# Optimization experiments

Measured on AMD Instinct MI355X. Metric: run time of the kernel, lower is better.

## Reference

```python
import jax, jax.numpy as jnp
import numpy as np

COMMITMENT_COST = 0.25


def setup_inputs() -> dict:
    key = jax.random.key(0)
    k1, k2 = jax.random.split(key)
    z = jax.random.normal(k1, (32, 256, 32, 32), dtype=jnp.float32)
    # codebook init matches torch uniform_(-1/codebook_size, 1/codebook_size)
    embedding = jax.random.uniform(k2, (1024, 256), dtype=jnp.float32,
                                   minval=-1.0 / 1024, maxval=1.0 / 1024)
    return {"z": z, "embedding": embedding}


def reference(z, embedding):
    # z: [B, C, H, W] -> [B, H, W, C]
    z_bhwc = jnp.transpose(z.astype(jnp.float32), (0, 2, 3, 1))
    B, H, W, C = z_bhwc.shape
    z_flat = z_bhwc.reshape(-1, C)                      # [N, C]

    # squared-distance matrix via norms + matmul: [N, K]
    d = (jnp.sum(z_flat ** 2, axis=1, keepdims=True)
         + jnp.sum(embedding ** 2, axis=1)
         - 2.0 * jnp.einsum('nc,kc->nk', z_flat, embedding))

    min_encoding_indices = jnp.argmin(d, axis=1)        # [N]
    z_quantized = embedding[min_encoding_indices].reshape(B, H, W, C)

    commitment_loss = COMMITMENT_COST * (jax.lax.stop_gradient(z_quantized) - z_bhwc) ** 2
    codebook_loss = (z_quantized - jax.lax.stop_gradient(z_bhwc)) ** 2
    loss = commitment_loss + codebook_loss              # [B, H, W, C]

    # straight-through estimator
    z_quantized = z_bhwc + jax.lax.stop_gradient(z_quantized - z_bhwc)
    z_quantized = jnp.transpose(z_quantized, (0, 3, 1, 2))  # [B, C, H, W]
    return z_quantized, loss, min_encoding_indices
```

## Files before the change

### kernel.cpp

```cpp
#include <hip/hip_runtime.h>

#define ZC     256
#define KCODES 1024
#define MARGIN 4e-4f
#define WIN    1e-4f

typedef __attribute__((ext_vector_type(4))) float f32x4;
typedef __attribute__((ext_vector_type(8))) short s16x8;
typedef unsigned int u32t;
typedef u32t __attribute__((address_space(1))) as1_u32;
typedef u32t __attribute__((address_space(3))) as3_u32;

__device__ __forceinline__ void glds16(const void* g, void* l) {
    __builtin_amdgcn_global_load_lds((const as1_u32*)g, (as3_u32*)l, 16, 0, 0);
}
__device__ __forceinline__ unsigned short bf16_rn(float x) {
    union { float f; u32t u; } v; v.f = x;
    return (unsigned short)((v.u + 0x7FFFu + ((v.u >> 16) & 1u)) >> 16);
}

__global__ __launch_bounds__(256)
void vq_prep_z(const float* __restrict__ z, unsigned short* __restrict__ Ab)
{
    const int t = threadIdx.x, blk = blockIdx.x;
    const int pt = (blk >> 3) * 64 + (t & 63);
    const int c0 = (blk & 7) * 32 + (t >> 6) * 8;
    const int b = pt >> 10, hw = pt & 1023;
    const float* zp = z + (size_t)b * (ZC * 1024) + (size_t)c0 * 1024 + hw;

    unsigned short hi[8];
    #pragma unroll
    for (int j = 0; j < 8; ++j) hi[j] = bf16_rn(zp[(size_t)j * 1024]);
    uint4 ph;
    ph.x = (u32t)hi[0] | ((u32t)hi[1] << 16); ph.y = (u32t)hi[2] | ((u32t)hi[3] << 16);
    ph.z = (u32t)hi[4] | ((u32t)hi[5] << 16); ph.w = (u32t)hi[6] | ((u32t)hi[7] << 16);

    const size_t kb = (size_t)(c0 >> 6);
    const int sw = (c0 & 63) ^ ((pt & 7) << 3);
    *reinterpret_cast<uint4*>(Ab + kb * (32768ull * 64) + (size_t)pt * 64 + sw) = ph;
}

__global__ __launch_bounds__(256)
void vq_prep_e(const float* __restrict__ emb, unsigned short* __restrict__ Bb)
{
    const int t = threadIdx.x, blk = blockIdx.x;
    const int code = (blk >> 3) * 64 + (t & 63);
    const int c0 = (blk & 7) * 32 + (t >> 6) * 8;
    const float* ep = emb + (size_t)code * ZC + c0;

    unsigned short hi[8];
    #pragma unroll
    for (int j = 0; j < 8; ++j) hi[j] = bf16_rn(ep[j]);
    uint4 ph;
    ph.x = (u32t)hi[0] | ((u32t)hi[1] << 16); ph.y = (u32t)hi[2] | ((u32t)hi[3] << 16);
    ph.z = (u32t)hi[4] | ((u32t)hi[5] << 16); ph.w = (u32t)hi[6] | ((u32t)hi[7] << 16);

    const size_t kb = (size_t)(c0 >> 6);
    const int sw = (c0 & 63) ^ ((code & 7) << 3);
    *reinterpret_cast<uint4*>(Bb + kb * (1024ull * 64) + (size_t)code * 64 + sw) = ph;
}

__global__ __launch_bounds__(256)
void vq_ens_np(const float* __restrict__ emb, float* __restrict__ ens_np,
               int* __restrict__ cnt)
{
    if (blockIdx.x == 0 && threadIdx.x == 0) *cnt = 0;
    const int t = threadIdx.x, g = t >> 3, r = t & 7;
    const int code = blockIdx.x * 32 + g;
    const float* er = emb + (size_t)code * ZC;

    float lo, hi;
    {
        const float a0 = er[r], a1 = er[128 + r];
        lo = __fmul_rn(a0, a0); hi = __fmul_rn(a1, a1);
    }
    #pragma unroll
    for (int i = 1; i < 16; ++i) {
        const int c = 8 * i + r;
        const float a0 = er[c], a1 = er[128 + c];
        lo = __fadd_rn(lo, __fmul_rn(a0, a0));
        hi = __fadd_rn(hi, __fmul_rn(a1, a1));
    }
    #pragma unroll
    for (int mk = 1; mk < 8; mk <<= 1) {
        lo = __fadd_rn(lo, __shfl_xor(lo, mk));
        hi = __fadd_rn(hi, __shfl_xor(hi, mk));
    }
    if (r == 0) ens_np[code] = __fadd_rn(lo, hi);
}

__global__ __launch_bounds__(256, 2)
void vq_gemm_argmin(const unsigned short* __restrict__ Ab,
                    const unsigned short* __restrict__ Bb,
                    const float* __restrict__ ens_g, float* __restrict__ out_idx)
{
    __shared__ unsigned short As[64 * 64];
    __shared__ unsigned short Bs[128 * 64];

    const int t = threadIdx.x;
    const int lane = t & 63, wv = t >> 6;
    const int col = lane & 15, kg = lane >> 4;
    const int pt0 = blockIdx.x * 64;
    const int kx = (col & 7) << 3;

    int aoff[4][2], boff[2][2];
    #pragma unroll
    for (int m = 0; m < 4; ++m)
        #pragma unroll
        for (int s = 0; s < 2; ++s)
            aoff[m][s] = (m * 16 + col) * 64 + ((s * 32 + kg * 8) ^ kx);
    #pragma unroll
    for (int n = 0; n < 2; ++n)
        #pragma unroll
        for (int s = 0; s < 2; ++s)
            boff[n][s] = (wv * 32 + n * 16 + col) * 64 + ((s * 32 + kg * 8) ^ kx);

    f32x4 acc[4][2];
    #pragma unroll
    for (int m = 0; m < 4; ++m)
        #pragma unroll
        for (int n = 0; n < 2; ++n) acc[m][n] = (f32x4){0.f, 0.f, 0.f, 0.f};

    float v1[16], v2[16]; int id1[16];
    #pragma unroll
    for (int i = 0; i < 16; ++i) { v1[i] = 3.4e38f; v2[i] = 3.4e38f; id1[i] = 0; }

    for (int ct = 0; ct < 8; ++ct) {
        for (int ks = 0; ks < 4; ++ks) {
            const char* aS = (const char*)(Ab + (size_t)ks * 2097152ull + (size_t)pt0 * 64);
            const char* bS = (const char*)(Bb + (size_t)ks * 65536ull + (size_t)ct * 8192);

            __syncthreads();
            glds16(aS + t * 16,        (char*)As + t * 16);
            glds16(aS + 4096 + t * 16, (char*)As + 4096 + t * 16);
            #pragma unroll
            for (int q = 0; q < 4; ++q)
                glds16(bS + q * 4096 + t * 16, (char*)Bs + q * 4096 + t * 16);
            __syncthreads();

            s16x8 af[4][2], bf[2][2];
            #pragma unroll
            for (int m = 0; m < 4; ++m)
                #pragma unroll
                for (int s = 0; s < 2; ++s)
                    af[m][s] = *reinterpret_cast<const s16x8*>(As + aoff[m][s]);
            #pragma unroll
            for (int n = 0; n < 2; ++n)
                #pragma unroll
                for (int s = 0; s < 2; ++s)
                    bf[n][s] = *reinterpret_cast<const s16x8*>(Bs + boff[n][s]);
            #pragma unroll
            for (int m = 0; m < 4; ++m)
                #pragma unroll
                for (int n = 0; n < 2; ++n) {
                    acc[m][n] = __builtin_amdgcn_mfma_f32_16x16x32_bf16(af[m][0], bf[n][0], acc[m][n], 0, 0, 0);
                    acc[m][n] = __builtin_amdgcn_mfma_f32_16x16x32_bf16(af[m][1], bf[n][1], acc[m][n], 0, 0, 0);
                }

            if (ks == 3) {
                #pragma unroll
                for (int n = 0; n < 2; ++n) {
                    const int code = ct * 128 + wv * 32 + n * 16 + col;
                    const float en = ens_g[code];
                    #pragma unroll
                    for (int m = 0; m < 4; ++m)
                        #pragma unroll
                        for (int j = 0; j < 4; ++j) {
                            const float sc = fmaf(-2.f, acc[m][n][j], en);
                            const int sl = m * 4 + j;
                            if (sc < v1[sl]) { v2[sl] = v1[sl]; v1[sl] = sc; id1[sl] = code; }
                            else if (sc < v2[sl]) { v2[sl] = sc; }
                            acc[m][n][j] = 0.f;
                        }
                }
            }
        }
    }

    float w1[16], w2[16]; int wid[16];
    #pragma unroll
    for (int sl = 0; sl < 16; ++sl) {
        float a1 = v1[sl]; int ai = id1[sl]; float a2 = v2[sl];
        #pragma unroll
        for (int mk = 1; mk < 16; mk <<= 1) {
            const float o1 = __shfl_xor(a1, mk);
            const int   oi = __shfl_xor(ai, mk);
            const float o2 = __shfl_xor(a2, mk);
            if (o1 < a1)      { a2 = fminf(a1, o2); a1 = o1; ai = oi; }
            else if (o1 > a1) { a2 = fminf(a2, o1); }
            else              { a2 = (oi != ai) ? a1 : fminf(a2, o2); ai = (oi < ai) ? oi : ai; }
        }
        w1[sl] = a1; w2[sl] = a2; wid[sl] = ai;
    }

    __syncthreads();
    float* mv1 = reinterpret_cast<float*>(As);
    float* mv2 = mv1 + 256;
    int*   mid = reinterpret_cast<int*>(mv2 + 256);
    if (col == 0) {
        #pragma unroll
        for (int sl = 0; sl < 16; ++sl) {
            const int m = sl >> 2, j = sl & 3;
            const int p = m * 16 + kg * 4 + j;
            mv1[wv * 64 + p] = w1[sl];
            mv2[wv * 64 + p] = w2[sl];
            mid[wv * 64 + p] = wid[sl];
        }
    }
    __syncthreads();
    if (t < 64) {
        float a1 = mv1[t], a2 = mv2[t]; int ai = mid[t];
        #pragma unroll
        for (int w = 1; w < 4; ++w) {
            const float b1 = mv1[w * 64 + t], b2 = mv2[w * 64 + t];
            const int   bi = mid[w * 64 + t];
            if (b1 < a1)      { a2 = fminf(a1, b2); a1 = b1; ai = bi; }
            else if (b1 > a1) { a2 = fminf(a2, b1); }
            else              { a2 = a1; ai = (bi < ai) ? bi : ai; }
        }
        out_idx[pt0 + t] = ((a2 - a1) <= MARGIN) ? (-1.0f - (float)ai) : (float)ai;
    }
}

__global__ __launch_bounds__(256)
void vq_compact(const float* __restrict__ idxf, int* __restrict__ cnt,
                int* __restrict__ list)
{
    const int n = blockIdx.x * 256 + threadIdx.x;
    if (idxf[n] < 0.f) { const int p = atomicAdd(cnt, 1); list[p] = n; }
}

__global__ __launch_bounds__(256, 1)
void vq_fixup6(const float* __restrict__ z, const float* __restrict__ emb,
               const float* __restrict__ ens_np, float* __restrict__ idxf,
               const int* __restrict__ cnt, const int* __restrict__ list)
{
    __shared__ float  zsb[4 * 264];
    __shared__ float  scr[4 * 1024];
    __shared__ float  znv[4];
    __shared__ float  smin[4];
    __shared__ int    pn[4];
    __shared__ float  redm[4];
    __shared__ int    candk[128];
    __shared__ int    candp[128];
    __shared__ int    ccnt;
    __shared__ double dred[4];
    __shared__ float  bestd_s[4];
    __shared__ int    bestk_s[4];

    const int t = threadIdx.x;
    const int g = t >> 3, r = t & 7;
    const int C = *cnt;
    const int base = blockIdx.x * 4;
    if (base >= C) return;
    const int npts = (C - base < 4) ? (C - base) : 4;

    if (t < 4) pn[t] = (base + t < C) ? list[base + t] : list[base];
    if (t == 0) ccnt = 0;
    __syncthreads();
    #pragma unroll
    for (int p = 0; p < 4; ++p) {
        const int n = pn[p];
        const int b = n >> 10, q = n & 1023;
        zsb[p * 264 + t] = z[(size_t)b * (ZC * 1024) + (size_t)t * 1024 + q];
    }
    __syncthreads();

    if (t < 32) {
        const float* zp = zsb + g * 264;
        float lo = __fmul_rn(zp[r], zp[r]);
        float hi = __fmul_rn(zp[128 + r], zp[128 + r]);
        #pragma unroll
        for (int i = 1; i < 16; ++i) {
            const int c = 8 * i + r;
            lo = __fadd_rn(lo, __fmul_rn(zp[c], zp[c]));
            hi = __fadd_rn(hi, __fmul_rn(zp[128 + c], zp[128 + c]));
        }
        #pragma unroll
        for (int mk = 1; mk < 8; mk <<= 1) {
            lo = __fadd_rn(lo, __shfl_xor(lo, mk));
            hi = __fadd_rn(hi, __shfl_xor(hi, mk));
        }
        if (r == 0) znv[g] = __fadd_rn(lo, hi);
    }

    const float* zb0 = zsb + 0 * 264 + r * 4;
    const float* zb1 = zsb + 1 * 264 + r * 4;
    const float* zb2 = zsb + 2 * 264 + r * 4;
    const float* zb3 = zsb + 3 * 264 + r * 4;

    float4 eA0, eA1, eA2, eA3, eA4, eA5, eA6, eA7;
    {
        const float* er = emb + (size_t)g * ZC + r * 4;
        eA0 = *reinterpret_cast<const float4*>(er);
        eA1 = *reinterpret_cast<const float4*>(er + 32);
        eA2 = *reinterpret_cast<const float4*>(er + 64);
        eA3 = *reinterpret_cast<const float4*>(er + 96);
        eA4 = *reinterpret_cast<const float4*>(er + 128);
        eA5 = *reinterpret_cast<const float4*>(er + 160);
        eA6 = *reinterpret_cast<const float4*>(er + 192);
        eA7 = *reinterpret_cast<const float4*>(er + 224);
    }

    for (int tile = 0; tile < 32; ++tile) {
        float4 eB0, eB1, eB2, eB3, eB4, eB5, eB6, eB7;
        if (tile < 31) {
            const float* er = emb + (size_t)(tile + 1) * 32 * ZC + (size_t)g * ZC + r * 4;
            eB0 = *reinterpret_cast<const float4*>(er);
            eB1 = *reinterpret_cast<const float4*>(er + 32);
            eB2 = *reinterpret_cast<const float4*>(er + 64);
            eB3 = *reinterpret_cast<const float4*>(er + 96);
            eB4 = *reinterpret_cast<const float4*>(er + 128);
            eB5 = *reinterpret_cast<const float4*>(er + 160);
            eB6 = *reinterpret_cast<const float4*>(er + 192);
            eB7 = *reinterpret_cast<const float4*>(er + 224);
        }

        float s0 = 0.f, s1 = 0.f, s2 = 0.f, s3 = 0.f;
        #define SCREEN_STEP(EV, OFF)                                           \
        {                                                                      \
            const float4 a0 = *reinterpret_cast<const float4*>(zb0 + (OFF));   \
            const float4 a1 = *reinterpret_cast<const float4*>(zb1 + (OFF));   \
            const float4 a2 = *reinterpret_cast<const float4*>(zb2 + (OFF));   \
            const float4 a3 = *reinterpret_cast<const float4*>(zb3 + (OFF));   \
            s0 = fmaf(EV.x, a0.x, s0); s0 = fmaf(EV.y, a0.y, s0);              \
            s0 = fmaf(EV.z, a0.z, s0); s0 = fmaf(EV.w, a0.w, s0);              \
            s1 = fmaf(EV.x, a1.x, s1); s1 = fmaf(EV.y, a1.y, s1);              \
            s1 = fmaf(EV.z, a1.z, s1); s1 = fmaf(EV.w, a1.w, s1);              \
            s2 = fmaf(EV.x, a2.x, s2); s2 = fmaf(EV.y, a2.y, s2);              \
            s2 = fmaf(EV.z, a2.z, s2); s2 = fmaf(EV.w, a2.w, s2);              \
            s3 = fmaf(EV.x, a3.x, s3); s3 = fmaf(EV.y, a3.y, s3);              \
            s3 = fmaf(EV.z, a3.z, s3); s3 = fmaf(EV.w, a3.w, s3);              \
        }
        SCREEN_STEP(eA0, 0)
        SCREEN_STEP(eA1, 32)
        SCREEN_STEP(eA2, 64)
        SCREEN_STEP(eA3, 96)
        SCREEN_STEP(eA4, 128)
        SCREEN_STEP(eA5, 160)
        SCREEN_STEP(eA6, 192)
        SCREEN_STEP(eA7, 224)
        #undef SCREEN_STEP

        #pragma unroll
        for (int mk = 1; mk < 8; mk <<= 1) {
            s0 += __shfl_xor(s0, mk);
            s1 += __shfl_xor(s1, mk);
            s2 += __shfl_xor(s2, mk);
            s3 += __shfl_xor(s3, mk);
        }
        if (r == 0) {
            const int code = tile * 32 + g;
            const float en = ens_np[code];
            scr[0 * 1024 + code] = fmaf(-2.f, s0, en);
            scr[1 * 1024 + code] = fmaf(-2.f, s1, en);
            scr[2 * 1024 + code] = fmaf(-2.f, s2, en);
            scr[3 * 1024 + code] = fmaf(-2.f, s3, en);
        }

        eA0 = eB0; eA1 = eB1; eA2 = eB2; eA3 = eB3;
        eA4 = eB4; eA5 = eB5; eA6 = eB6; eA7 = eB7;
    }
    __syncthreads();

    for (int p = 0; p < 4; ++p) {
        float m = fminf(fminf(scr[p * 1024 + t],       scr[p * 1024 + t + 256]),
                        fminf(scr[p * 1024 + t + 512], scr[p * 1024 + t + 768]));
        #pragma unroll
        for (int mk = 1; mk < 64; mk <<= 1) m = fminf(m, __shfl_xor(m, mk));
        if ((t & 63) == 0) redm[t >> 6] = m;
        __syncthreads();
        if (t == 0) smin[p] = fminf(fminf(redm[0], redm[1]), fminf(redm[2], redm[3]));
        __syncthreads();
    }

    for (int p = 0; p < 4; ++p) {
        #pragma unroll
        for (int rep = 0; rep < 4; ++rep) {
            const int code = rep * 256 + t;
            if (scr[p * 1024 + code] <= smin[p] + WIN) {
                const int pos = atomicAdd(&ccnt, 1);
                if (pos < 128) { candk[pos] = code; candp[pos] = p; }
            }
        }
    }
    __syncthreads();
    const int NC = (ccnt < 128) ? ccnt : 128;

    if (t < 4) { bestd_s[t] = 3.4e38f; bestk_s[t] = 0x7fffffff; }
    __syncthreads();
    for (int ci = 0; ci < NC; ++ci) {
        const int code = candk[ci], p = candp[ci];
        double dd = (double)emb[(size_t)code * ZC + t] * (double)zsb[p * 264 + t];
        #pragma unroll
        for (int mk = 1; mk < 64; mk <<= 1) dd = dd + __shfl_xor(dd, mk);
        if ((t & 63) == 0) dred[t >> 6] = dd;
        __syncthreads();
        if (t == 0) {
            const double tot = (dred[0] + dred[1]) + (dred[2] + dred[3]);
            const float t2f = (float)tot;
            const float d = __fsub_rn(__fadd_rn(znv[p], ens_np[code]),
                                      __fmul_rn(2.0f, t2f));
            if (d < bestd_s[p] || (d == bestd_s[p] && code < bestk_s[p])) {
                bestd_s[p] = d; bestk_s[p] = code;
            }
        }
        __syncthreads();
    }
    if (t < npts) idxf[pn[t]] = (float)bestk_s[t];
}

__global__ __launch_bounds__(256)
void vq_outputs_kernel(const float* __restrict__ z, const float* __restrict__ emb,
                       const float* __restrict__ idxf,
                       float* __restrict__ out_q, float* __restrict__ out_loss)
{
    __shared__ float zts[32 * 257];
    __shared__ int   ids[32];

    const int t  = threadIdx.x;
    const int bh = blockIdx.x;
    const int b  = bh >> 5, h = bh & 31;
    const int n0 = bh * 32;

    if (t < 32) ids[t] = (int)idxf[n0 + t];
    __syncthreads();

    const size_t zbase = (size_t)b * (ZC * 1024) + h * 32;

    for (int rep = 0; rep < 32; ++rep) {
        const int flat = rep * 256 + t;
        const int c = flat >> 5;
        const int ww = flat & 31;
        const size_t ga = zbase + (size_t)c * 1024 + ww;
        const float zv = z[ga];
        zts[ww * 257 + c] = zv;
        out_q[ga] = emb[(size_t)ids[ww] * ZC + c];
    }
    __syncthreads();

    for (int rep = 0; rep < 32; ++rep) {
        const float e = emb[(size_t)ids[rep] * ZC + t];
        const float d = e - zts[rep * 257 + t];
        out_loss[(size_t)(n0 + rep) * ZC + t] = 1.25f * d * d;
    }
}

extern "C" void kernel_launch(void* const* d_in, const int* in_sizes, int n_in,
                              void* d_out, int out_size, void* d_ws, size_t ws_size,
                              hipStream_t stream)
{
    const float* z   = (const float*)d_in[0];
    const float* emb = (const float*)d_in[1];
    float* out      = (float*)d_out;
    float* out_q    = out;
    float* out_loss = out + 8388608;
    float* out_idx  = out + 16777216;

    unsigned short* Ab = (unsigned short*)d_out;
    unsigned short* Bb = (unsigned short*)((char*)d_out + 33554432);
    float* ensg = (float*)((char*)d_out + 34603008);
    int*   cnt  = (int*)  ((char*)d_out + 34607104);
    int*   list = (int*)  ((char*)d_out + 34607168);

    vq_prep_z        <<<4096, 256, 0, stream>>>(z, Ab);
    vq_prep_e        <<<128,  256, 0, stream>>>(emb, Bb);
    vq_ens_np        <<<32,   256, 0, stream>>>(emb, ensg, cnt);
    vq_gemm_argmin   <<<512,  256, 0, stream>>>(Ab, Bb, ensg, out_idx);
    vq_compact       <<<128,  256, 0, stream>>>(out_idx, cnt, list);
    vq_fixup6        <<<8192, 256, 0, stream>>>(z, emb, ensg, out_idx, cnt, list);
    vq_outputs_kernel<<<1024, 256, 0, stream>>>(z, emb, out_idx, out_q, out_loss);
}
```

Baseline: 187.5 us.

## Split GEMM-argmin over codebook halves and merge partial top-2 results

The fused GEMM+argmin kernel now launches twice as many blocks, each covering half the codebook (4 of 8 code tiles) for a 64-point tile. Each block writes its partial best, second-best and index to workspace, and a new merge kernel combines the two halves and applies the margin flag. The aim is better occupancy across the GPU's compute units, since 512 blocks may underfill the device. The cost is one extra kernel launch, extra global traffic for the partials, and each A tile being loaded twice.

Measured after the change: 196.8 us. +5.0%, slower.

```diff
diff --git a/kernel.cpp b/kernel.cpp
--- a/kernel.cpp
+++ b/kernel.cpp
@@ -4,6 +4,7 @@
 #define KCODES 1024
 #define MARGIN 4e-4f
 #define WIN    1e-4f
+#define NPT    32768
 
 typedef __attribute__((ext_vector_type(4))) float f32x4;
 typedef __attribute__((ext_vector_type(8))) short s16x8;
@@ -92,7 +93,9 @@
 __global__ __launch_bounds__(256, 2)
 void vq_gemm_argmin(const unsigned short* __restrict__ Ab,
                     const unsigned short* __restrict__ Bb,
-                    const float* __restrict__ ens_g, float* __restrict__ out_idx)
+                    const float* __restrict__ ens_g,
+                    float* __restrict__ partV1, float* __restrict__ partV2,
+                    int* __restrict__ partI)
 {
     __shared__ unsigned short As[64 * 64];
     __shared__ unsigned short Bs[128 * 64];
@@ -100,7 +103,9 @@
     const int t = threadIdx.x;
     const int lane = t & 63, wv = t >> 6;
     const int col = lane & 15, kg = lane >> 4;
-    const int pt0 = blockIdx.x * 64;
+    const int blk = blockIdx.x;
+    const int pt0 = (blk >> 1) * 64;
+    const int half = blk & 1;
     const int kx = (col & 7) << 3;
 
     int aoff[4][2], boff[2][2];
@@ -125,7 +130,8 @@
     #pragma unroll
     for (int i = 0; i < 16; ++i) { v1[i] = 3.4e38f; v2[i] = 3.4e38f; id1[i] = 0; }
 
-    for (int ct = 0; ct < 8; ++ct) {
+    for (int ci = 0; ci < 4; ++ci) {
+        const int ct = half * 4 + ci;
         for (int ks = 0; ks < 4; ++ks) {
             const char* aS = (const char*)(Ab + (size_t)ks * 2097152ull + (size_t)pt0 * 64);
             const char* bS = (const char*)(Bb + (size_t)ks * 65536ull + (size_t)ct * 8192);
@@ -218,8 +224,25 @@
             else if (b1 > a1) { a2 = fminf(a2, b1); }
             else              { a2 = a1; ai = (bi < ai) ? bi : ai; }
         }
-        out_idx[pt0 + t] = ((a2 - a1) <= MARGIN) ? (-1.0f - (float)ai) : (float)ai;
-    }
+        const int g = half * NPT + pt0 + t;
+        partV1[g] = a1; partV2[g] = a2; partI[g] = ai;
+    }
+}
+
+__global__ __launch_bounds__(256)
+void vq_merge(const float* __restrict__ partV1, const float* __restrict__ partV2,
+              const int* __restrict__ partI, float* __restrict__ out_idx)
+{
+    const int n = blockIdx.x * 256 + threadIdx.x;
+    const float a1 = partV1[n],       a2 = partV2[n];
+    const int   ai = partI[n];
+    const float b1 = partV1[NPT + n], b2 = partV2[NPT + n];
+    const int   bi = partI[NPT + n];
+    float v1f, v2f; int idf;
+    if (b1 < a1)      { v1f = b1; idf = bi; v2f = fminf(a1, b2); }
+    else if (b1 > a1) { v1f = a1; idf = ai; v2f = fminf(a2, b1); }
+    else              { v1f = a1; idf = (bi < ai) ? bi : ai; v2f = a1; }
+    out_idx[n] = ((v2f - v1f) <= MARGIN) ? (-1.0f - (float)idf) : (float)idf;
 }
 
 __global__ __launch_bounds__(256)
@@ -462,11 +485,15 @@
     float* ensg = (float*)((char*)d_out + 34603008);
     int*   cnt  = (int*)  ((char*)d_out + 34607104);
     int*   list = (int*)  ((char*)d_out + 34607168);
+    float* pV1  = (float*)((char*)d_out + 34738240);
+    float* pV2  = (float*)((char*)d_out + 35000384);
+    int*   pI   = (int*)  ((char*)d_out + 35262528);
 
     vq_prep_z        <<<4096, 256, 0, stream>>>(z, Ab);
     vq_prep_e        <<<128,  256, 0, stream>>>(emb, Bb);
     vq_ens_np        <<<32,   256, 0, stream>>>(emb, ensg, cnt);
-    vq_gemm_argmin   <<<512,  256, 0, stream>>>(Ab, Bb, ensg, out_idx);
+    vq_gemm_argmin   <<<1024, 256, 0, stream>>>(Ab, Bb, ensg, pV1, pV2, pI);
+    vq_merge         <<<128,  256, 0, stream>>>(pV1, pV2, pI, out_idx);
     vq_compact       <<<128,  256, 0, stream>>>(out_idx, cnt, list);
     vq_fixup6        <<<8192, 256, 0, stream>>>(z, emb, ensg, out_idx, cnt, list);
     vq_outputs_kernel<<<1024, 256, 0, stream>>>(z, emb, out_idx, out_q, out_loss);
```
